# Kernel optimization log

Hardware: AMD Instinct MI355X
Metric: run time of the kernel (lower is better)

Reference implementation:

```python
import jax, jax.numpy as jnp
import numpy as np

LR, HR = 1024, 2048
H1, D1 = 8, (2 * HR) // 8   # feature_learner: heads=8, head_dim=512, out=2*HR
H2, D2 = 4, HR // 4          # upsampler: heads=4, head_dim=512, out=HR
EPS = 1e-5


def _graph_norm(h, gamma, beta, mscale):
    # PyG GraphNorm over a single graph: mean/var across the node dimension.
    mean = h.mean(axis=0, keepdims=True)
    out = h - mscale * mean
    var = (out * out).mean(axis=0, keepdims=True)
    return gamma * out * jax.lax.rsqrt(var + EPS) + beta


def _l2norm_rows(h):
    return h / jnp.linalg.norm(h, axis=1, keepdims=True)


def _transformer_conv(x, Wq, bq, Wk, bk, Wv, bv, Wskip, bskip, H, D, We=None, e=None):
    # PyG TransformerConv on a complete graph (with self-loops) == dense MHA
    # with optional scalar edge feature e[i, j] embedded via We and added to
    # key and value, plus a root/skip linear term.
    N = x.shape[0]
    Q = (x @ Wq + bq).reshape(N, H, D)
    K = (x @ Wk + bk).reshape(N, H, D)
    V = (x @ Wv + bv).reshape(N, H, D)
    scores = jnp.einsum('ihd,jhd->hij', Q, K)  # [H, N, N]
    if We is not None:
        Weh = We.reshape(H, D)                              # edge embedding dirs
        qe = jnp.einsum('ihd,hd->hi', Q, Weh)               # q_i . We per head
        scores = scores + qe[:, :, None] * e[None]          # + e_ij * (q.We)
    alpha = jax.nn.softmax(scores / jnp.sqrt(jnp.float32(D)), axis=2)
    out = jnp.einsum('hij,jhd->ihd', alpha, V)              # [N, H, D]
    if We is not None:
        ae = jnp.einsum('hij,ij->ih', alpha, e)             # sum_j alpha*e_ij
        out = out + ae[:, :, None] * Weh[None]
    return out.reshape(N, H * D) + x @ Wskip + bskip


def setup_inputs() -> dict:
    key = jax.random.key(0)
    ks = jax.random.split(key, 24)
    s_in = 1.0 / np.sqrt(LR)
    s_e = 1.0

    def p(k, shape, scale):
        return (jax.random.normal(k, shape, jnp.float32) * scale)

    F1 = H1 * D1  # 4096
    F2 = H2 * D2  # 2048
    return {
        'x': jax.random.normal(ks[0], (LR, LR), jnp.float32),
        # conv1 (feature_learner): in=LR, out=F1, edge_dim=1
        'Wq1': p(ks[1], (LR, F1), s_in), 'bq1': jnp.zeros((F1,), jnp.float32),
        'Wk1': p(ks[2], (LR, F1), s_in), 'bk1': jnp.zeros((F1,), jnp.float32),
        'Wv1': p(ks[3], (LR, F1), s_in), 'bv1': jnp.zeros((F1,), jnp.float32),
        'We1': p(ks[4], (1, F1), s_e),
        'Wskip1': p(ks[5], (LR, F1), s_in), 'bskip1': jnp.zeros((F1,), jnp.float32),
        'g1': jnp.ones((F1,), jnp.float32), 'bb1': jnp.zeros((F1,), jnp.float32),
        'ms1': jnp.ones((F1,), jnp.float32),
        # conv2 (upsampler): in=LR, out=F2, no edge features
        'Wq2': p(ks[6], (LR, F2), s_in), 'bq2': jnp.zeros((F2,), jnp.float32),
        'Wk2': p(ks[7], (LR, F2), s_in), 'bk2': jnp.zeros((F2,), jnp.float32),
        'Wv2': p(ks[8], (LR, F2), s_in), 'bv2': jnp.zeros((F2,), jnp.float32),
        'Wskip2': p(ks[9], (LR, F2), s_in), 'bskip2': jnp.zeros((F2,), jnp.float32),
        'g2': jnp.ones((F2,), jnp.float32), 'bb2': jnp.zeros((F2,), jnp.float32),
        'ms2': jnp.ones((F2,), jnp.float32),
    }


def reference(x, Wq1, bq1, Wk1, bk1, Wv1, bv1, We1, Wskip1, bskip1, g1, bb1, ms1,
              Wq2, bq2, Wk2, bk2, Wv2, bv2, Wskip2, bskip2, g2, bb2, ms2):
    # feature learner: edge_attr = x.view(-1,1), edge (src=j, dst=i) carries x[j, i]
    h1 = _transformer_conv(x, Wq1, bq1, Wk1, bk1, Wv1, bv1, Wskip1, bskip1,
                           H1, D1, We=We1, e=x.T)
    h1 = _graph_norm(h1, g1, bb1, ms1)
    lr_x = _l2norm_rows(h1)                      # [LR, 2*HR]
    # upsampler: nodes are the 2*HR columns of lr_x
    h2 = _transformer_conv(lr_x.T, Wq2, bq2, Wk2, bk2, Wv2, bv2, Wskip2, bskip2,
                           H2, D2)               # [2*HR, HR]
    hr_x = _graph_norm(h2, g2, bb2, ms2).T       # [HR, 2*HR]
    hr_x = _l2norm_rows(hr_x)
    hr = jax.nn.relu(hr_x @ hr_x.T)              # [HR, HR]
    return (hr, jax.nn.relu(lr_x @ lr_x.T))
```

## Files before the change

### kernel.cpp

```cpp
#include <hip/hip_runtime.h>
#include <hip/hip_bf16.h>

typedef unsigned short u16;
typedef __attribute__((ext_vector_type(8))) short bf16x8;
typedef __attribute__((ext_vector_type(4))) float f32x4;

__device__ __constant__ float kInvSqrtD = 0.04419417382415922f;

__device__ __forceinline__ u16 f2bf(float f) {
  union { float f; unsigned u; } a; a.f = f;
  unsigned r = a.u + 0x7FFFu + ((a.u >> 16) & 1u);
  return (u16)(r >> 16);
}
__device__ __forceinline__ float bf2f(u16 u) {
  union { unsigned u; float f; } a; a.u = ((unsigned)u) << 16;
  return a.f;
}

__device__ __forceinline__ float blockReduceMax(float v, float* red) {
  int tid = threadIdx.x;
  red[tid] = v; __syncthreads();
  #pragma unroll
  for (int w = 128; w > 0; w >>= 1) {
    if (tid < w) red[tid] = fmaxf(red[tid], red[tid + w]);
    __syncthreads();
  }
  float r = red[0];
  __syncthreads();
  return r;
}
__device__ __forceinline__ float blockReduceSum(float v, float* red) {
  int tid = threadIdx.x;
  red[tid] = v; __syncthreads();
  #pragma unroll
  for (int w = 128; w > 0; w >>= 1) {
    if (tid < w) red[tid] = red[tid] + red[tid + w];
    __syncthreads();
  }
  float r = red[0];
  __syncthreads();
  return r;
}

__device__ __forceinline__ float4 blockReduceF4(float4 v, float4* red) {
  int tid = threadIdx.x;
  red[tid] = v; __syncthreads();
  #pragma unroll
  for (int w = 128; w > 0; w >>= 1) {
    if (tid < w) {
      float4 a = red[tid], b = red[tid + w];
      a.x += b.x; a.y += b.y; a.z += b.z; a.w += b.w;
      red[tid] = a;
    }
    __syncthreads();
  }
  float4 r = red[0];
  __syncthreads();
  return r;
}

#define GLDS16(gp, lp)                                                         \
  __builtin_amdgcn_global_load_lds(                                            \
      (const __attribute__((address_space(1))) void*)(gp),                     \
      (__attribute__((address_space(3))) void*)(lp), 16, 0, 0)

__device__ __forceinline__ void xcd_map(int gx, int gy, int& bx, int& by) {
  const int nwg = gx * gy;
  const int orig = blockIdx.y * gx + blockIdx.x;
  if ((nwg & 7) == 0) {
    int bestfx = 0, bestcost = 1 << 30;
    #pragma unroll
    for (int fx = 1; fx <= 8; fx <<= 1) {
      int fy = 8 / fx;
      if ((gx % fx) == 0 && (gy % fy) == 0) {
        int cost = gx / fx + gy / fy;
        if (cost < bestcost) { bestcost = cost; bestfx = fx; }
      }
    }
    if (bestfx > 0) {
      const int fx = bestfx, fy = 8 / bestfx;
      const int rw = gx / fx, rh = gy / fy;
      const int xcd = orig & 7, lid = orig >> 3;
      bx = (xcd % fx) * rw + lid % rw;
      by = (xcd / fx) * rh + lid / rw;
      return;
    }
    const int q = nwg >> 3;
    const int xcd = orig & 7, lid = orig >> 3;
    const int wgid = xcd * q + lid;
    bx = wgid % gx; by = wgid / gx;
    return;
  }
  const int q = nwg >> 3, r = nwg & 7;
  const int xcd = orig & 7, lid = orig >> 3;
  const int wgid = (xcd < r ? xcd * (q + 1) : r * (q + 1) + (xcd - r) * q) + lid;
  bx = wgid % gx; by = wgid / gx;
}

template<int OUTM, bool ACCUM, bool RELU, bool RANK1, bool BIAS>
__global__ __launch_bounds__(512) void mgemm8_k(
    const u16* __restrict__ A, int lda, long long sA,
    const u16* __restrict__ B, int ldb, long long sB,
    const float* __restrict__ bias, int sBias,
    float* __restrict__ Cf, u16* __restrict__ Cb, int ldc, long long sC,
    int K,
    const float* __restrict__ r1row, int sR1r,
    const float* __restrict__ r1col, int sR1c)
{
  __shared__ u16 smem[8 * 8192];
  const int z = blockIdx.z;
  const u16* Ag = A + (long long)z * sA;
  const u16* Bg = B + (long long)z * sB;

  int bx, by;
  xcd_map(gridDim.x, gridDim.y, bx, by);

  const int row0 = by << 7;
  const int col0 = bx << 7;
  const int tid  = threadIdx.x;
  const int lane = tid & 63;
  const int w    = tid >> 6;
  const int g    = w >> 2;
  const int s4   = w & 3;
  const int wr   = (s4 >> 1) << 6;
  const int wc   = (s4 & 1) << 6;

  const int srow = tid >> 2;
  const int ssw  = (tid & 3) ^ ((srow >> 1) & 3);
  const long long aoff = (long long)(row0 + srow) * lda + ssw * 8;
  const long long boff = (long long)(col0 + srow) * ldb + ssw * 8;

  const int frow = lane & 15;
  const int fsw  = (lane >> 4) ^ ((frow >> 1) & 3);
  const int fAoff = ((wr + frow) << 5) + (fsw << 3);
  const int fBoff = ((wc + frow) << 5) + (fsw << 3);

#define STAGE8(tt) do {                                                        \
    u16* _sb = smem + (((tt) & 7) << 13);                                      \
    const long long _k = (long long)(tt) << 5;                                 \
    GLDS16(Ag + aoff + _k, _sb + (tid << 3));                                  \
    GLDS16(Bg + boff + _k, _sb + 4096 + (tid << 3));                           \
  } while (0)

  f32x4 acc[4][4];
  #pragma unroll
  for (int mi = 0; mi < 4; ++mi)
    #pragma unroll
    for (int ni = 0; ni < 4; ++ni) {
      acc[mi][ni][0] = 0.f; acc[mi][ni][1] = 0.f;
      acc[mi][ni][2] = 0.f; acc[mi][ni][3] = 0.f;
    }

  const int NT = K >> 5;
  const int NP = NT >> 1;
  STAGE8(0); STAGE8(1); STAGE8(2); STAGE8(3); STAGE8(4); STAGE8(5);
  asm volatile("s_waitcnt vmcnt(8)" ::: "memory");
  __builtin_amdgcn_s_barrier();
  asm volatile("" ::: "memory");

  for (int i = 0; i < NP; ++i) {
    if (i + 3 < NP) { STAGE8(2 * i + 6); STAGE8(2 * i + 7); }

    const u16* base = smem + (((2 * i + g) & 7) << 13);
    bf16x8 af[4], bfr[4];
    #pragma unroll
    for (int mi = 0; mi < 4; ++mi) af[mi]  = *(const bf16x8*)(base + fAoff + mi * 512);
    #pragma unroll
    for (int ni = 0; ni < 4; ++ni) bfr[ni] = *(const bf16x8*)(base + 4096 + fBoff + ni * 512);
    __builtin_amdgcn_s_setprio(1);
    #pragma unroll
    for (int mi = 0; mi < 4; ++mi)
      #pragma unroll
      for (int ni = 0; ni < 4; ++ni)
        acc[mi][ni] = __builtin_amdgcn_mfma_f32_16x16x32_bf16(
            af[mi], bfr[ni], acc[mi][ni], 0, 0, 0);
    __builtin_amdgcn_s_setprio(0);

    if (i + 1 < NP) {
      if (i + 3 < NP)      asm volatile("s_waitcnt vmcnt(8)" ::: "memory");
      else if (i + 2 < NP) asm volatile("s_waitcnt vmcnt(4)" ::: "memory");
      else                 asm volatile("s_waitcnt vmcnt(0)" ::: "memory");
      __builtin_amdgcn_s_barrier();
      asm volatile("" ::: "memory");
    }
  }
#undef STAGE8

  float* dump = (float*)smem;
  if (w >= 4) {
    float* reg = dump + ((w - 4) << 12);
    #pragma unroll
    for (int f = 0; f < 16; ++f) {
      int mi = f >> 2, ni = f & 3;
      *(f32x4*)(reg + (lane << 6) + (((f + lane) & 15) << 2)) = acc[mi][ni];
    }
  }
  asm volatile("s_waitcnt lgkmcnt(0)" ::: "memory");
  __builtin_amdgcn_s_barrier();
  asm volatile("" ::: "memory");
  if (w < 4) {
    float* reg = dump + (w << 12);
    #pragma unroll
    for (int f = 0; f < 16; ++f) {
      int mi = f >> 2, ni = f & 3;
      acc[mi][ni] += *(const f32x4*)(reg + (lane << 6) + (((f + lane) & 15) << 2));
    }
  }
  asm volatile("s_waitcnt lgkmcnt(0)" ::: "memory");
  __builtin_amdgcn_s_barrier();
  asm volatile("" ::: "memory");

  float* tile = (float*)smem;
  if (w < 4) {
    const int cn  = lane & 15;
    const int rm4 = (lane >> 4) << 2;
    #pragma unroll
    for (int mi = 0; mi < 4; ++mi) {
      #pragma unroll
      for (int ni = 0; ni < 4; ++ni) {
        const int rl = wr + mi * 16 + rm4;
        const int cl = wc + ni * 16 + cn;
        if (OUTM == 2) {
          *(f32x4*)&tile[cl * 132 + rl] = acc[mi][ni];
        } else {
          #pragma unroll
          for (int j = 0; j < 4; ++j) tile[(rl + j) * 132 + cl] = acc[mi][ni][j];
        }
      }
    }
  }
  asm volatile("s_waitcnt lgkmcnt(0)" ::: "memory");
  __builtin_amdgcn_s_barrier();
  asm volatile("" ::: "memory");

  #pragma unroll
  for (int p = 0; p < 8; ++p) {
    const int rr = p * 16 + (tid >> 5);
    const int c4 = (tid & 31) << 2;
    f32x4 v = *(const f32x4*)&tile[rr * 132 + c4];
    if (OUTM == 2) {
      const int cc = col0 + rr;
      float badd = BIAS ? bias[(long long)z * sBias + cc] : 0.f;
      u16* pp = Cb + (long long)z * sC + (long long)cc * ldc + row0 + c4;
      ushort4 o;
      o.x = f2bf(v[0] + badd); o.y = f2bf(v[1] + badd);
      o.z = f2bf(v[2] + badd); o.w = f2bf(v[3] + badd);
      *(ushort4*)pp = o;
    } else {
      const int R = row0 + rr;
      const long long idx = (long long)z * sC + (long long)R * ldc + col0 + c4;
      float val[4] = {v[0], v[1], v[2], v[3]};
      if (BIAS) {
        float4 b4 = *(const float4*)&bias[(long long)z * sBias + col0 + c4];
        val[0] += b4.x; val[1] += b4.y; val[2] += b4.z; val[3] += b4.w;
      }
      if (RANK1) {
        float rr1 = r1row[(long long)z * sR1r + R];
        float4 c4v = *(const float4*)&r1col[(long long)z * sR1c + col0 + c4];
        val[0] += rr1 * c4v.x; val[1] += rr1 * c4v.y;
        val[2] += rr1 * c4v.z; val[3] += rr1 * c4v.w;
      }
      if (OUTM == 0) {
        if (ACCUM) {
          float4 old = *(const float4*)&Cf[idx];
          val[0] += old.x; val[1] += old.y; val[2] += old.z; val[3] += old.w;
        }
        if (RELU) {
          val[0] = fmaxf(val[0], 0.f); val[1] = fmaxf(val[1], 0.f);
          val[2] = fmaxf(val[2], 0.f); val[3] = fmaxf(val[3], 0.f);
        }
        float4 o4; o4.x = val[0]; o4.y = val[1]; o4.z = val[2]; o4.w = val[3];
        *(float4*)&Cf[idx] = o4;
      } else {
        ushort4 o;
        o.x = f2bf(val[0]); o.y = f2bf(val[1]);
        o.z = f2bf(val[2]); o.w = f2bf(val[3]);
        *(ushort4*)&Cb[idx] = o;
      }
    }
  }
}

template<bool BIAS>
__global__ __launch_bounds__(512, 2) void mgemm256_k(
    const u16* __restrict__ A, int lda, long long sA,
    const u16* __restrict__ B, int ldb, long long sB,
    const float* __restrict__ bias, int sBias,
    u16* __restrict__ Cb, int ldc, long long sC,
    int K)
{
  __shared__ u16 smem[4 * 16384];
  const int z = blockIdx.z;
  const u16* Ag = A + (long long)z * sA;
  const u16* Bg = B + (long long)z * sB;

  int bx, by;
  xcd_map(gridDim.x, gridDim.y, bx, by);

  const int row0 = bx << 8;
  const int dummy = 0; (void)dummy;
  const int row0r = by << 8;
  const int col0 = bx << 8;
  (void)row0;
  const int tid  = threadIdx.x;
  const int lane = tid & 63;
  const int w    = tid >> 6;
  const int wrow = w >> 2;
  const int wcol = w & 3;

  const int srow = tid >> 2;
  const int ssw  = (tid & 3) ^ ((srow >> 1) & 3);
  const long long aoff0 = (long long)(row0r + srow)       * lda + ssw * 8;
  const long long aoff1 = (long long)(row0r + srow + 128) * lda + ssw * 8;
  const long long boff0 = (long long)(col0 + srow)        * ldb + ssw * 8;
  const long long boff1 = (long long)(col0 + srow + 128)  * ldb + ssw * 8;

  const int frow = lane & 15;
  const int fsw  = (lane >> 4) ^ ((frow >> 1) & 3);
  const int fAoff = ((wrow * 128 + frow) << 5) + (fsw << 3);
  const int fBoff = ((wcol * 64  + frow) << 5) + (fsw << 3);

#define STG256(tt) do {                                                        \
    u16* _sb = smem + (((tt) & 3) << 14);                                      \
    const long long _k = (long long)(tt) << 5;                                 \
    GLDS16(Ag + aoff0 + _k, _sb + (tid << 3));                                 \
    GLDS16(Ag + aoff1 + _k, _sb + 4096 + (tid << 3));                          \
    GLDS16(Bg + boff0 + _k, _sb + 8192 + (tid << 3));                          \
    GLDS16(Bg + boff1 + _k, _sb + 12288 + (tid << 3));                         \
  } while (0)

  f32x4 acc[8][4];
  #pragma unroll
  for (int mi = 0; mi < 8; ++mi)
    #pragma unroll
    for (int ni = 0; ni < 4; ++ni) {
      acc[mi][ni][0] = 0.f; acc[mi][ni][1] = 0.f;
      acc[mi][ni][2] = 0.f; acc[mi][ni][3] = 0.f;
    }

  const int NT = K >> 5;
  STG256(0); STG256(1); STG256(2);
  asm volatile("s_waitcnt vmcnt(8)" ::: "memory");
  __builtin_amdgcn_s_barrier();
  asm volatile("" ::: "memory");

  for (int t = 0; t < NT; ++t) {
    if (t + 3 < NT) STG256(t + 3);

    const u16* base = smem + ((t & 3) << 14);
    bf16x8 af[8], bfr[4];
    #pragma unroll
    for (int mi = 0; mi < 8; ++mi) af[mi]  = *(const bf16x8*)(base + fAoff + mi * 512);
    #pragma unroll
    for (int ni = 0; ni < 4; ++ni) bfr[ni] = *(const bf16x8*)(base + 8192 + fBoff + ni * 512);
    __builtin_amdgcn_s_setprio(1);
    #pragma unroll
    for (int mi = 0; mi < 8; ++mi)
      #pragma unroll
      for (int ni = 0; ni < 4; ++ni)
        acc[mi][ni] = __builtin_amdgcn_mfma_f32_16x16x32_bf16(
            af[mi], bfr[ni], acc[mi][ni], 0, 0, 0);
    __builtin_amdgcn_s_setprio(0);

    if (t + 1 < NT) {
      if (t + 3 < NT)      asm volatile("s_waitcnt vmcnt(8)" ::: "memory");
      else if (t + 2 < NT) asm volatile("s_waitcnt vmcnt(4)" ::: "memory");
      else                 asm volatile("s_waitcnt vmcnt(0)" ::: "memory");
      __builtin_amdgcn_s_barrier();
      asm volatile("" ::: "memory");
    }
  }
#undef STG256

  const int cn  = lane & 15;
  const int rm4 = (lane >> 4) << 2;
  #pragma unroll
  for (int mi = 0; mi < 8; ++mi) {
    #pragma unroll
    for (int ni = 0; ni < 4; ++ni) {
      const int rb = row0r + wrow * 128 + mi * 16 + rm4;
      const int cc = col0 + wcol * 64 + ni * 16 + cn;
      float badd = BIAS ? bias[(long long)z * sBias + cc] : 0.f;
      f32x4 v = acc[mi][ni];
      #pragma unroll
      for (int j = 0; j < 4; ++j)
        Cb[(long long)z * sC + (long long)(rb + j) * ldc + cc] = f2bf(v[j] + badd);
    }
  }
}

__global__ __launch_bounds__(256) void reduce4relu_k(
    const float* __restrict__ p, float* __restrict__ out, int n4)
{
  int i = blockIdx.x * 256 + threadIdx.x;
  if (i < n4) {
    float4 a = ((const float4*)p)[i];
    float4 b = ((const float4*)(p + (1ll << 20)))[i];
    float4 c = ((const float4*)(p + (2ll << 20)))[i];
    float4 d = ((const float4*)(p + (3ll << 20)))[i];
    float4 o;
    o.x = fmaxf(a.x + b.x + c.x + d.x, 0.f);
    o.y = fmaxf(a.y + b.y + c.y + d.y, 0.f);
    o.z = fmaxf(a.z + b.z + c.z + d.z, 0.f);
    o.w = fmaxf(a.w + b.w + c.w + d.w, 0.f);
    ((float4*)out)[i] = o;
  }
}

__global__ __launch_bounds__(256) void xpose_k(
    const float* __restrict__ in, float* __restrict__ out, int R, int Cc)
{
  __shared__ float tile[32][33];
  int c0 = blockIdx.x * 32, r0 = blockIdx.y * 32;
  int tx = threadIdx.x & 31, ty = threadIdx.x >> 5;
  #pragma unroll
  for (int rr = ty; rr < 32; rr += 8)
    tile[rr][tx] = in[(long long)(r0 + rr) * Cc + c0 + tx];
  __syncthreads();
  #pragma unroll
  for (int cc = ty; cc < 32; cc += 8)
    out[(long long)(c0 + cc) * R + r0 + tx] = tile[tx][cc];
}

__global__ __launch_bounds__(256) void tcvt_k(
    const float* __restrict__ in, u16* __restrict__ out, int R, int Cc)
{
  __shared__ float tile[32][33];
  int c0 = blockIdx.x * 32, r0 = blockIdx.y * 32;
  int tx = threadIdx.x & 31, ty = threadIdx.x >> 5;
  #pragma unroll
  for (int rr = ty; rr < 32; rr += 8)
    tile[rr][tx] = in[(long long)(r0 + rr) * Cc + c0 + tx];
  __syncthreads();
  #pragma unroll
  for (int cc = ty; cc < 32; cc += 8)
    out[(long long)(c0 + cc) * R + r0 + tx] = f2bf(tile[tx][cc]);
}

__global__ __launch_bounds__(256) void tcvt_aff_k(
    const float* __restrict__ in, u16* __restrict__ out, int R, int Cc,
    const float* __restrict__ A2, const float* __restrict__ C2)
{
  __shared__ float tile[32][33];
  int c0 = blockIdx.x * 32, r0 = blockIdx.y * 32;
  int tx = threadIdx.x & 31, ty = threadIdx.x >> 5;
  #pragma unroll
  for (int rr = ty; rr < 32; rr += 8)
    tile[rr][tx] = in[(long long)(r0 + rr) * Cc + c0 + tx];
  __syncthreads();
  #pragma unroll
  for (int cc = ty; cc < 32; cc += 8) {
    float v = A2[c0 + cc] * tile[tx][cc] + C2[c0 + cc];
    out[(long long)(c0 + cc) * R + r0 + tx] = f2bf(v);
  }
}

__global__ __launch_bounds__(256) void cvt_k(
    const float* __restrict__ in, u16* __restrict__ out)
{
  int i = blockIdx.x * 256 + threadIdx.x;
  float4 v = ((const float4*)in)[i];
  ushort4 o;
  o.x = f2bf(v.x); o.y = f2bf(v.y); o.z = f2bf(v.z); o.w = f2bf(v.w);
  ((ushort4*)out)[i] = o;
}

__global__ __launch_bounds__(256) void pack2_k(
    const float* __restrict__ a, const float* __restrict__ b,
    float* __restrict__ out, int n)
{
  int i = blockIdx.x * 256 + threadIdx.x;
  if (i < n) { out[i] = a[i]; out[n + i] = b[i]; }
}

__global__ __launch_bounds__(64) void qe_k(const u16* __restrict__ Q1,
                                           const float* __restrict__ We1,
                                           float* __restrict__ qe)
{
  int h = blockIdx.x >> 10;
  int i = blockIdx.x & 1023;
  const u16* q = Q1 + (long long)i * 4096 + h * 512;
  const float* wv = We1 + h * 512;
  int l = threadIdx.x;
  float s = 0.f;
  #pragma unroll
  for (int r = 0; r < 8; ++r) s += bf2f(q[l + r * 64]) * wv[l + r * 64];
  #pragma unroll
  for (int off = 32; off > 0; off >>= 1) s += __shfl_down(s, off);
  if (l == 0) qe[blockIdx.x] = s;
}

__global__ __launch_bounds__(256) void softmax1b_k(
    u16* __restrict__ S, const float* __restrict__ xT,
    const float* __restrict__ qe, float* __restrict__ ae)
{
  int i = blockIdx.x, h = blockIdx.y;
  u16* s = S + ((long long)h * 1024 + i) * 1024;
  const float* e = xT + (long long)i * 1024;
  float q = qe[h * 1024 + i];
  int tid = threadIdx.x;
  __shared__ float red[256];

  ushort4 sv = ((const ushort4*)s)[tid];
  float4  evv = ((const float4*)e)[tid];
  float ev[4] = {evv.x, evv.y, evv.z, evv.w};
  float t[4];
  t[0] = (bf2f(sv.x) + q * ev[0]) * kInvSqrtD;
  t[1] = (bf2f(sv.y) + q * ev[1]) * kInvSqrtD;
  t[2] = (bf2f(sv.z) + q * ev[2]) * kInvSqrtD;
  t[3] = (bf2f(sv.w) + q * ev[3]) * kInvSqrtD;
  float m = fmaxf(fmaxf(t[0], t[1]), fmaxf(t[2], t[3]));
  m = blockReduceMax(m, red);
  float sum = 0.f;
  #pragma unroll
  for (int r = 0; r < 4; ++r) { t[r] = __expf(t[r] - m); sum += t[r]; }
  sum = blockReduceSum(sum, red);
  float invl = 1.f / sum;
  float aes = 0.f;
  ushort4 o;
  o.x = f2bf(t[0] * invl); o.y = f2bf(t[1] * invl);
  o.z = f2bf(t[2] * invl); o.w = f2bf(t[3] * invl);
  #pragma unroll
  for (int r = 0; r < 4; ++r) aes += (t[r] * invl) * ev[r];
  ((ushort4*)s)[tid] = o;
  aes = blockReduceSum(aes, red);
  if (tid == 0) ae[h * 1024 + i] = aes;
}

__global__ __launch_bounds__(256) void softmax2b_k(u16* __restrict__ S)
{
  u16* s = S + ((long long)blockIdx.y * 2048 + blockIdx.x) * 4096;
  int tid = threadIdx.x;
  __shared__ float red[256];
  float t[16];
  float m = -1e30f;
  #pragma unroll
  for (int r = 0; r < 4; ++r) {
    ushort4 sv = ((const ushort4*)s)[tid + r * 256];
    t[r*4+0] = bf2f(sv.x) * kInvSqrtD; t[r*4+1] = bf2f(sv.y) * kInvSqrtD;
    t[r*4+2] = bf2f(sv.z) * kInvSqrtD; t[r*4+3] = bf2f(sv.w) * kInvSqrtD;
    m = fmaxf(m, fmaxf(fmaxf(t[r*4], t[r*4+1]), fmaxf(t[r*4+2], t[r*4+3])));
  }
  m = blockReduceMax(m, red);
  float sum = 0.f;
  #pragma unroll
  for (int r = 0; r < 16; ++r) { t[r] = __expf(t[r] - m); sum += t[r]; }
  sum = blockReduceSum(sum, red);
  float invl = 1.f / sum;
  #pragma unroll
  for (int r = 0; r < 4; ++r) {
    ushort4 o;
    o.x = f2bf(t[r*4+0] * invl); o.y = f2bf(t[r*4+1] * invl);
    o.z = f2bf(t[r*4+2] * invl); o.w = f2bf(t[r*4+3] * invl);
    ((ushort4*)s)[tid + r * 256] = o;
  }
}

__global__ __launch_bounds__(256) void colpart4_k(const float* __restrict__ h,
    int N, int F, int nchunk, float* __restrict__ ps, float* __restrict__ pss)
{
  const int f4 = blockIdx.x * 256 + threadIdx.x;
  const int chunk = blockIdx.y;
  const int rows = N / nchunk;
  const int rbeg = chunk * rows;
  const int F4 = F >> 2;
  const float4* h4 = (const float4*)h;
  float4 s = {0.f, 0.f, 0.f, 0.f}, ss = {0.f, 0.f, 0.f, 0.f};
  #pragma unroll 8
  for (int i = 0; i < rows; ++i) {
    float4 v = h4[(long long)(rbeg + i) * F4 + f4];
    s.x += v.x; s.y += v.y; s.z += v.z; s.w += v.w;
    ss.x += v.x * v.x; ss.y += v.y * v.y;
    ss.z += v.z * v.z; ss.w += v.w * v.w;
  }
  ((float4*)(ps  + (long long)chunk * F))[f4] = s;
  ((float4*)(pss + (long long)chunk * F))[f4] = ss;
}

template<int MODE>
__global__ __launch_bounds__(256) void colfin2_k(
    const float* __restrict__ ps, const float* __restrict__ pss,
    int F, int nchunk, float Nf,
    const float* __restrict__ ms, const float* __restrict__ g,
    const float* __restrict__ beta,
    float* __restrict__ outA, float* __restrict__ outC)
{
  __shared__ float4 red4[256];
  const int f4 = blockIdx.x;
  const int tid = threadIdx.x;
  float4 s = {0.f, 0.f, 0.f, 0.f}, ss = {0.f, 0.f, 0.f, 0.f};
  for (int c = tid; c < nchunk; c += 256) {
    float4 v = ((const float4*)(ps  + (long long)c * F))[f4];
    float4 u = ((const float4*)(pss + (long long)c * F))[f4];
    s.x += v.x; s.y += v.y; s.z += v.z; s.w += v.w;
    ss.x += u.x; ss.y += u.y; ss.z += u.z; ss.w += u.w;
  }
  s  = blockReduceF4(s, red4);
  ss = blockReduceF4(ss, red4);
  if (tid < 4) {
    const int f = f4 * 4 + tid;
    float sv  = (tid == 0) ? s.x  : (tid == 1) ? s.y  : (tid == 2) ? s.z  : s.w;
    float ssv = (tid == 0) ? ss.x : (tid == 1) ? ss.y : (tid == 2) ? ss.z : ss.w;
    float Ninv = 1.f / Nf;
    float mean = sv * Ninv;
    float mm = ms[f] * mean;
    float var = ssv * Ninv - 2.f * mm * mean + mm * mm;
    float is = rsqrtf(var + 1e-5f);
    float a = g[f] * is;
    float c = beta[f] - a * mm;
    if (MODE == 1) {
      float sy2 = a * a * ssv + 2.f * a * c * sv + Nf * c * c;
      float cinv = rsqrtf(sy2);
      a *= cinv; c *= cinv;
    }
    outA[f] = a;
    outC[f] = c;
  }
}

__global__ __launch_bounds__(256) void rowl2gn_k(
    float* __restrict__ h, u16* __restrict__ hb,
    const float* __restrict__ a, const float* __restrict__ c)
{
  int i = blockIdx.x;
  float* row = h + (long long)i * 4096;
  u16* rb = hb + (long long)i * 4096;
  int tid = threadIdx.x;
  __shared__ float red[256];
  float t[16];
  float ss = 0.f;
  #pragma unroll
  for (int r = 0; r < 4; ++r) {
    int j = tid + r * 256;
    float4 hv = ((const float4*)row)[j];
    float4 av = ((const float4*)a)[j];
    float4 cv = ((const float4*)c)[j];
    t[r*4+0] = av.x * hv.x + cv.x;
    t[r*4+1] = av.y * hv.y + cv.y;
    t[r*4+2] = av.z * hv.z + cv.z;
    t[r*4+3] = av.w * hv.w + cv.w;
    ss += t[r*4+0]*t[r*4+0] + t[r*4+1]*t[r*4+1]
        + t[r*4+2]*t[r*4+2] + t[r*4+3]*t[r*4+3];
  }
  ss = blockReduceSum(ss, red);
  float inv = rsqrtf(ss);
  #pragma unroll
  for (int r = 0; r < 4; ++r) {
    int j = tid + r * 256;
    float4 o4;
    o4.x = t[r*4+0] * inv; o4.y = t[r*4+1] * inv;
    o4.z = t[r*4+2] * inv; o4.w = t[r*4+3] * inv;
    ((float4*)row)[j] = o4;
    ushort4 ob;
    ob.x = f2bf(o4.x); ob.y = f2bf(o4.y); ob.z = f2bf(o4.z); ob.w = f2bf(o4.w);
    ((ushort4*)rb)[j] = ob;
  }
}

extern "C" void kernel_launch(void* const* d_in, const int* in_sizes, int n_in,
                              void* d_out, int out_size, void* d_ws, size_t ws_size,
                              hipStream_t stream)
{
  (void)in_sizes; (void)n_in; (void)out_size; (void)ws_size;

  const float* x      = (const float*)d_in[0];
  const float* Wq1    = (const float*)d_in[1];
  const float* bq1    = (const float*)d_in[2];
  const float* Wk1    = (const float*)d_in[3];
  const float* bk1    = (const float*)d_in[4];
  const float* Wv1    = (const float*)d_in[5];
  const float* bv1    = (const float*)d_in[6];
  const float* We1    = (const float*)d_in[7];
  const float* Wskip1 = (const float*)d_in[8];
  const float* bskip1 = (const float*)d_in[9];
  const float* g1     = (const float*)d_in[10];
  const float* bb1    = (const float*)d_in[11];
  const float* ms1    = (const float*)d_in[12];
  const float* Wq2    = (const float*)d_in[13];
  const float* bq2    = (const float*)d_in[14];
  const float* Wk2    = (const float*)d_in[15];
  const float* bk2    = (const float*)d_in[16];
  const float* Wv2    = (const float*)d_in[17];
  const float* bv2    = (const float*)d_in[18];
  const float* Wskip2 = (const float*)d_in[19];
  const float* bskip2 = (const float*)d_in[20];
  const float* g2     = (const float*)d_in[21];
  const float* bb2    = (const float*)d_in[22];
  const float* ms2    = (const float*)d_in[23];

  char* base = (char*)d_ws;
  float* lrx_f   = (float*)(base);
  u16*   lrx_bf  = (u16*)  (base + (16ll << 20));
  u16*   lrxT_bf = (u16*)  (base + (24ll << 20));
  u16*   hrx_bf  = (u16*)  (base + (32ll << 20));
  char* sh = base + (48ll << 20);
  u16* x_bf  = (u16*)(sh);
  float* xT  = (float*)(sh + (2ll << 20));
  u16* Wq1T  = (u16*)(sh + (6ll << 20));
  u16* Wk1T  = (u16*)(sh + (14ll << 20));
  u16* Wv1T  = (u16*)(sh + (22ll << 20));
  u16* Ws1T  = (u16*)(sh + (30ll << 20));
  u16* Q1bf  = (u16*)(sh + (38ll << 20));
  u16* K1bf  = (u16*)(sh + (46ll << 20));
  u16* V1T   = (u16*)(sh + (54ll << 20));
  u16* S1bf  = (u16*)(sh + (62ll << 20));
  float* ps1  = (float*)(sh + (66ll << 20));
  float* pss1 = (float*)(sh + (68ll << 20));
  u16* Wq2T  = (u16*)(sh);
  u16* Wk2T  = (u16*)(sh + (4ll << 20));
  u16* Wv2T  = (u16*)(sh + (8ll << 20));
  u16* Ws2T  = (u16*)(sh + (12ll << 20));
  u16* Q2bf  = (u16*)(sh + (16ll << 20));
  u16* K2bf  = (u16*)(sh + (32ll << 20));
  u16* V2T   = (u16*)(sh + (48ll << 20));
  float* H2  = (float*)(sh + (64ll << 20));
  u16* S2bf  = (u16*)(sh + (96ll << 20));
  float* gpart = (float*)(sh + (96ll << 20));
  float* ps2  = (float*)(sh + (120ll << 20));
  float* pss2 = (float*)(sh + (122ll << 20));
  float* tail    = (float*)(base + (208ll << 20));
  float* qe      = tail;
  float* ae      = qe + 8192;
  float* af1     = ae + 8192;
  float* cf1     = af1 + 4096;
  float* A2v     = cf1 + 4096;
  float* C2v     = A2v + 2048;
  float* biasQK1 = C2v + 2048;
  float* biasQK2 = biasQK1 + 8192;

  float* out0 = (float*)d_out;
  float* out1 = out0 + (long long)2048 * 2048;

  xpose_k<<<dim3(32, 32), 256, 0, stream>>>(x, xT, 1024, 1024);
  cvt_k<<<dim3(1024), 256, 0, stream>>>(x, x_bf);
  tcvt_k<<<dim3(128, 32), 256, 0, stream>>>(Wq1,    Wq1T, 1024, 4096);
  tcvt_k<<<dim3(128, 32), 256, 0, stream>>>(Wk1,    Wk1T, 1024, 4096);
  tcvt_k<<<dim3(128, 32), 256, 0, stream>>>(Wv1,    Wv1T, 1024, 4096);
  tcvt_k<<<dim3(128, 32), 256, 0, stream>>>(Wskip1, Ws1T, 1024, 4096);
  pack2_k<<<dim3(16), 256, 0, stream>>>(bq1, bk1, biasQK1, 4096);
  pack2_k<<<dim3(8),  256, 0, stream>>>(bq2, bk2, biasQK2, 2048);

  mgemm8_k<1,false,false,false,true><<<dim3(32, 8, 2), 512, 0, stream>>>(
      x_bf, 1024, 0, Wq1T, 1024, (long long)4096 * 1024, biasQK1, 4096,
      nullptr, Q1bf, 4096, (long long)1024 * 4096, 1024, nullptr, 0, nullptr, 0);
  mgemm8_k<2,false,false,false,true><<<dim3(32, 8, 1), 512, 0, stream>>>(
      x_bf, 1024, 0, Wv1T, 1024, 0, bv1, 0, nullptr, V1T, 1024, 0, 1024,
      nullptr, 0, nullptr, 0);
  mgemm8_k<0,false,false,false,true><<<dim3(32, 8, 1), 512, 0, stream>>>(
      x_bf, 1024, 0, Ws1T, 1024, 0, bskip1, 0, lrx_f, nullptr, 4096, 0, 1024,
      nullptr, 0, nullptr, 0);

  qe_k<<<dim3(8192), 64, 0, stream>>>(Q1bf, We1, qe);

  mgemm8_k<1,false,false,false,false><<<dim3(8, 8, 8), 512, 0, stream>>>(
      Q1bf, 4096, 512, K1bf, 4096, 512, nullptr, 0, nullptr, S1bf, 1024, 1048576,
      512, nullptr, 0, nullptr, 0);

  softmax1b_k<<<dim3(1024, 8), 256, 0, stream>>>(S1bf, xT, qe, ae);

  mgemm8_k<0,true,false,true,false><<<dim3(4, 8, 8), 512, 0, stream>>>(
      S1bf, 1024, 1048576, V1T, 1024, 512 * 1024, nullptr, 0, lrx_f, nullptr,
      4096, 512, 1024, ae, 1024, We1, 512);

  colpart4_k<<<dim3(4, 128), 256, 0, stream>>>(lrx_f, 1024, 4096, 128, ps1, pss1);
  colfin2_k<0><<<dim3(1024), 256, 0, stream>>>(ps1, pss1, 4096, 128, 1024.f,
                                               ms1, g1, bb1, af1, cf1);
  rowl2gn_k<<<dim3(1024), 256, 0, stream>>>(lrx_f, lrx_bf, af1, cf1);
  tcvt_k<<<dim3(128, 32), 256, 0, stream>>>(lrx_f, lrxT_bf, 1024, 4096);

  tcvt_k<<<dim3(64, 32), 256, 0, stream>>>(Wq2,    Wq2T, 1024, 2048);
  tcvt_k<<<dim3(64, 32), 256, 0, stream>>>(Wk2,    Wk2T, 1024, 2048);
  tcvt_k<<<dim3(64, 32), 256, 0, stream>>>(Wv2,    Wv2T, 1024, 2048);
  tcvt_k<<<dim3(64, 32), 256, 0, stream>>>(Wskip2, Ws2T, 1024, 2048);

  mgemm256_k<true><<<dim3(8, 16, 2), 512, 0, stream>>>(
      lrxT_bf, 1024, 0, Wq2T, 1024, (long long)2048 * 1024, biasQK2, 2048,
      Q2bf, 2048, (long long)4096 * 2048, 1024);
  mgemm8_k<2,false,false,false,true><<<dim3(16, 32, 1), 512, 0, stream>>>(
      lrxT_bf, 1024, 0, Wv2T, 1024, 0, bv2, 0, nullptr, V2T, 4096, 0, 1024,
      nullptr, 0, nullptr, 0);
  mgemm8_k<0,false,false,false,true><<<dim3(16, 32, 1), 512, 0, stream>>>(
      lrxT_bf, 1024, 0, Ws2T, 1024, 0, bskip2, 0, H2, nullptr, 2048, 0, 1024,
      nullptr, 0, nullptr, 0);

  for (int c = 0; c < 2; ++c) {
    const u16* Qc = Q2bf + (long long)c * 2048 * 2048;
    float* Hc = H2 + (long long)c * 2048 * 2048;
    mgemm256_k<false><<<dim3(16, 8, 4), 512, 0, stream>>>(
        Qc, 2048, 512, K2bf, 2048, 512, nullptr, 0,
        S2bf, 4096, (long long)2048 * 4096, 512);
    softmax2b_k<<<dim3(2048, 4), 256, 0, stream>>>(S2bf);
    mgemm8_k<0,true,false,false,false><<<dim3(4, 16, 4), 512, 0, stream>>>(
        S2bf, 4096, (long long)2048 * 4096, V2T, 4096, (long long)512 * 4096,
        nullptr, 0, Hc, nullptr, 2048, 512, 4096, nullptr, 0, nullptr, 0);
  }

  colpart4_k<<<dim3(2, 256), 256, 0, stream>>>(H2, 4096, 2048, 256, ps2, pss2);
  colfin2_k<1><<<dim3(512), 256, 0, stream>>>(ps2, pss2, 2048, 256, 4096.f,
                                              ms2, g2, bb2, A2v, C2v);
  tcvt_aff_k<<<dim3(64, 128), 256, 0, stream>>>(H2, hrx_bf, 4096, 2048, A2v, C2v);

  mgemm8_k<0,false,true,false,false><<<dim3(16, 16, 1), 512, 0, stream>>>(
      hrx_bf, 4096, 0, hrx_bf, 4096, 0, nullptr, 0, out0, nullptr, 2048, 0, 4096,
      nullptr, 0, nullptr, 0);
  mgemm8_k<0,false,false,false,false><<<dim3(8, 8, 4), 512, 0, stream>>>(
      lrx_bf, 4096, 1024, lrx_bf, 4096, 1024, nullptr, 0, gpart, nullptr, 1024,
      (long long)1 << 20, 1024, nullptr, 0, nullptr, 0);
  reduce4relu_k<<<dim3(1024), 256, 0, stream>>>(gpart, out1, 262144);
}
```

Measured before the change: 644.3 us.

## Shrink GEMM shared-memory rings to raise occupancy with double-barrier pipelining

Both GEMM kernels now keep fewer shared-memory stages: 4 stages instead of 8 for the 128-tile kernel and 2 instead of 4 for the 256-tile kernel. Each now declares launch_bounds(512,4) so more workgroups can be resident per CU. The loop reads fragments into registers first, then hits a second barrier, then issues the next global-to-LDS loads so they overlap the MFMAs. The epilogue is factored into a shared helper. In exchange there is a shallower prefetch depth, an extra barrier per iteration, and a tighter register budget that may cause spills.

```diff
diff --git a/kernel.cpp b/kernel.cpp
--- a/kernel.cpp
+++ b/kernel.cpp
@@ -98,94 +98,13 @@
 }
 
 template<int OUTM, bool ACCUM, bool RELU, bool RANK1, bool BIAS>
-__global__ __launch_bounds__(512) void mgemm8_k(
-    const u16* __restrict__ A, int lda, long long sA,
-    const u16* __restrict__ B, int ldb, long long sB,
-    const float* __restrict__ bias, int sBias,
-    float* __restrict__ Cf, u16* __restrict__ Cb, int ldc, long long sC,
-    int K,
-    const float* __restrict__ r1row, int sR1r,
-    const float* __restrict__ r1col, int sR1c)
-{
-  __shared__ u16 smem[8 * 8192];
-  const int z = blockIdx.z;
-  const u16* Ag = A + (long long)z * sA;
-  const u16* Bg = B + (long long)z * sB;
-
-  int bx, by;
-  xcd_map(gridDim.x, gridDim.y, bx, by);
-
-  const int row0 = by << 7;
-  const int col0 = bx << 7;
-  const int tid  = threadIdx.x;
-  const int lane = tid & 63;
-  const int w    = tid >> 6;
-  const int g    = w >> 2;
-  const int s4   = w & 3;
-  const int wr   = (s4 >> 1) << 6;
-  const int wc   = (s4 & 1) << 6;
-
-  const int srow = tid >> 2;
-  const int ssw  = (tid & 3) ^ ((srow >> 1) & 3);
-  const long long aoff = (long long)(row0 + srow) * lda + ssw * 8;
-  const long long boff = (long long)(col0 + srow) * ldb + ssw * 8;
-
-  const int frow = lane & 15;
-  const int fsw  = (lane >> 4) ^ ((frow >> 1) & 3);
-  const int fAoff = ((wr + frow) << 5) + (fsw << 3);
-  const int fBoff = ((wc + frow) << 5) + (fsw << 3);
-
-#define STAGE8(tt) do {                                                        \
-    u16* _sb = smem + (((tt) & 7) << 13);                                      \
-    const long long _k = (long long)(tt) << 5;                                 \
-    GLDS16(Ag + aoff + _k, _sb + (tid << 3));                                  \
-    GLDS16(Bg + boff + _k, _sb + 4096 + (tid << 3));                           \
-  } while (0)
-
-  f32x4 acc[4][4];
-  #pragma unroll
-  for (int mi = 0; mi < 4; ++mi)
-    #pragma unroll
-    for (int ni = 0; ni < 4; ++ni) {
-      acc[mi][ni][0] = 0.f; acc[mi][ni][1] = 0.f;
-      acc[mi][ni][2] = 0.f; acc[mi][ni][3] = 0.f;
-    }
-
-  const int NT = K >> 5;
-  const int NP = NT >> 1;
-  STAGE8(0); STAGE8(1); STAGE8(2); STAGE8(3); STAGE8(4); STAGE8(5);
-  asm volatile("s_waitcnt vmcnt(8)" ::: "memory");
-  __builtin_amdgcn_s_barrier();
-  asm volatile("" ::: "memory");
-
-  for (int i = 0; i < NP; ++i) {
-    if (i + 3 < NP) { STAGE8(2 * i + 6); STAGE8(2 * i + 7); }
-
-    const u16* base = smem + (((2 * i + g) & 7) << 13);
-    bf16x8 af[4], bfr[4];
-    #pragma unroll
-    for (int mi = 0; mi < 4; ++mi) af[mi]  = *(const bf16x8*)(base + fAoff + mi * 512);
-    #pragma unroll
-    for (int ni = 0; ni < 4; ++ni) bfr[ni] = *(const bf16x8*)(base + 4096 + fBoff + ni * 512);
-    __builtin_amdgcn_s_setprio(1);
-    #pragma unroll
-    for (int mi = 0; mi < 4; ++mi)
-      #pragma unroll
-      for (int ni = 0; ni < 4; ++ni)
-        acc[mi][ni] = __builtin_amdgcn_mfma_f32_16x16x32_bf16(
-            af[mi], bfr[ni], acc[mi][ni], 0, 0, 0);
-    __builtin_amdgcn_s_setprio(0);
-
-    if (i + 1 < NP) {
-      if (i + 3 < NP)      asm volatile("s_waitcnt vmcnt(8)" ::: "memory");
-      else if (i + 2 < NP) asm volatile("s_waitcnt vmcnt(4)" ::: "memory");
-      else                 asm volatile("s_waitcnt vmcnt(0)" ::: "memory");
-      __builtin_amdgcn_s_barrier();
-      asm volatile("" ::: "memory");
-    }
-  }
-#undef STAGE8
-
+__device__ __forceinline__ void epilogue128(
+    u16* smem, f32x4 (&acc)[4][4],
+    int z, int row0, int col0, int tid, int lane, int w, int wr, int wc,
+    const float* bias, int sBias,
+    float* Cf, u16* Cb, int ldc, long long sC,
+    const float* r1row, int sR1r, const float* r1col, int sR1c)
+{
   float* dump = (float*)smem;
   if (w >= 4) {
     float* reg = dump + ((w - 4) << 12);
@@ -281,15 +200,107 @@
   }
 }
 
+template<int OUTM, bool ACCUM, bool RELU, bool RANK1, bool BIAS>
+__global__ __launch_bounds__(512, 4) void mgemm8d_k(
+    const u16* __restrict__ A, int lda, long long sA,
+    const u16* __restrict__ B, int ldb, long long sB,
+    const float* __restrict__ bias, int sBias,
+    float* __restrict__ Cf, u16* __restrict__ Cb, int ldc, long long sC,
+    int K,
+    const float* __restrict__ r1row, int sR1r,
+    const float* __restrict__ r1col, int sR1c)
+{
+  __shared__ u16 smem[33792];
+  const int z = blockIdx.z;
+  const u16* Ag = A + (long long)z * sA;
+  const u16* Bg = B + (long long)z * sB;
+
+  int bx, by;
+  xcd_map(gridDim.x, gridDim.y, bx, by);
+
+  const int row0 = by << 7;
+  const int col0 = bx << 7;
+  const int tid  = threadIdx.x;
+  const int lane = tid & 63;
+  const int w    = tid >> 6;
+  const int g    = w >> 2;
+  const int s4   = w & 3;
+  const int wr   = (s4 >> 1) << 6;
+  const int wc   = (s4 & 1) << 6;
+
+  const int srow = tid >> 2;
+  const int ssw  = (tid & 3) ^ ((srow >> 1) & 3);
+  const long long aoff = (long long)(row0 + srow) * lda + ssw * 8;
+  const long long boff = (long long)(col0 + srow) * ldb + ssw * 8;
+
+  const int frow = lane & 15;
+  const int fsw  = (lane >> 4) ^ ((frow >> 1) & 3);
+  const int fAoff = ((wr + frow) << 5) + (fsw << 3);
+  const int fBoff = ((wc + frow) << 5) + (fsw << 3);
+
+#define STAGE4(tt) do {                                                        \
+    u16* _sb = smem + (((tt) & 3) << 13);                                      \
+    const long long _k = (long long)(tt) << 5;                                 \
+    GLDS16(Ag + aoff + _k, _sb + (tid << 3));                                  \
+    GLDS16(Bg + boff + _k, _sb + 4096 + (tid << 3));                           \
+  } while (0)
+
+  f32x4 acc[4][4];
+  #pragma unroll
+  for (int mi = 0; mi < 4; ++mi)
+    #pragma unroll
+    for (int ni = 0; ni < 4; ++ni) {
+      acc[mi][ni][0] = 0.f; acc[mi][ni][1] = 0.f;
+      acc[mi][ni][2] = 0.f; acc[mi][ni][3] = 0.f;
+    }
+
+  const int NT = K >> 5;
+  const int NP = NT >> 1;
+  STAGE4(0); STAGE4(1); STAGE4(2); STAGE4(3);
+
+  for (int p = 0; p < NP; ++p) {
+    if (p + 1 < NP) asm volatile("s_waitcnt vmcnt(4)" ::: "memory");
+    else            asm volatile("s_waitcnt vmcnt(0)" ::: "memory");
+    __builtin_amdgcn_s_barrier();
+    asm volatile("" ::: "memory");
+
+    const u16* base = smem + (((2 * p + g) & 3) << 13);
+    bf16x8 af[4], bfr[4];
+    #pragma unroll
+    for (int mi = 0; mi < 4; ++mi) af[mi]  = *(const bf16x8*)(base + fAoff + mi * 512);
+    #pragma unroll
+    for (int ni = 0; ni < 4; ++ni) bfr[ni] = *(const bf16x8*)(base + 4096 + fBoff + ni * 512);
+    asm volatile("s_waitcnt lgkmcnt(0)" ::: "memory");
+    __builtin_amdgcn_s_barrier();
+    asm volatile("" ::: "memory");
+
+    if (p + 2 < NP) { STAGE4(2 * p + 4); STAGE4(2 * p + 5); }
+
+    __builtin_amdgcn_s_setprio(1);
+    #pragma unroll
+    for (int mi = 0; mi < 4; ++mi)
+      #pragma unroll
+      for (int ni = 0; ni < 4; ++ni)
+        acc[mi][ni] = __builtin_amdgcn_mfma_f32_16x16x32_bf16(
+            af[mi], bfr[ni], acc[mi][ni], 0, 0, 0);
+    __builtin_amdgcn_s_setprio(0);
+  }
+#undef STAGE4
+
+  epilogue128<OUTM, ACCUM, RELU, RANK1, BIAS>(
+      smem, acc, z, row0, col0, tid, lane, w, wr, wc,
+      bias, sBias, Cf, Cb, ldc, sC, r1row, sR1r, r1col, sR1c);
+}
+
 template<bool BIAS>
-__global__ __launch_bounds__(512, 2) void mgemm256_k(
+__global__ __launch_bounds__(512, 4) void mgemm256d_k(
     const u16* __restrict__ A, int lda, long long sA,
     const u16* __restrict__ B, int ldb, long long sB,
     const float* __restrict__ bias, int sBias,
     u16* __restrict__ Cb, int ldc, long long sC,
     int K)
 {
-  __shared__ u16 smem[4 * 16384];
+  __shared__ u16 smem[2 * 16384];
   const int z = blockIdx.z;
   const u16* Ag = A + (long long)z * sA;
   const u16* Bg = B + (long long)z * sB;
@@ -297,11 +308,8 @@
   int bx, by;
   xcd_map(gridDim.x, gridDim.y, bx, by);
 
-  const int row0 = bx << 8;
-  const int dummy = 0; (void)dummy;
   const int row0r = by << 8;
   const int col0 = bx << 8;
-  (void)row0;
   const int tid  = threadIdx.x;
   const int lane = tid & 63;
   const int w    = tid >> 6;
@@ -321,7 +329,7 @@
   const int fBoff = ((wcol * 64  + frow) << 5) + (fsw << 3);
 
 #define STG256(tt) do {                                                        \
-    u16* _sb = smem + (((tt) & 3) << 14);                                      \
+    u16* _sb = smem + (((tt) & 1) << 14);                                      \
     const long long _k = (long long)(tt) << 5;                                 \
     GLDS16(Ag + aoff0 + _k, _sb + (tid << 3));                                 \
     GLDS16(Ag + aoff1 + _k, _sb + 4096 + (tid << 3));                          \
@@ -339,20 +347,26 @@
     }
 
   const int NT = K >> 5;
-  STG256(0); STG256(1); STG256(2);
-  asm volatile("s_waitcnt vmcnt(8)" ::: "memory");
-  __builtin_amdgcn_s_barrier();
-  asm volatile("" ::: "memory");
+  STG256(0); STG256(1);
 
   for (int t = 0; t < NT; ++t) {
-    if (t + 3 < NT) STG256(t + 3);
-
-    const u16* base = smem + ((t & 3) << 14);
+    if (t + 1 < NT) asm volatile("s_waitcnt vmcnt(4)" ::: "memory");
+    else            asm volatile("s_waitcnt vmcnt(0)" ::: "memory");
+    __builtin_amdgcn_s_barrier();
+    asm volatile("" ::: "memory");
+
+    const u16* base = smem + ((t & 1) << 14);
     bf16x8 af[8], bfr[4];
     #pragma unroll
     for (int mi = 0; mi < 8; ++mi) af[mi]  = *(const bf16x8*)(base + fAoff + mi * 512);
     #pragma unroll
     for (int ni = 0; ni < 4; ++ni) bfr[ni] = *(const bf16x8*)(base + 8192 + fBoff + ni * 512);
+    asm volatile("s_waitcnt lgkmcnt(0)" ::: "memory");
+    __builtin_amdgcn_s_barrier();
+    asm volatile("" ::: "memory");
+
+    if (t + 2 < NT) STG256(t + 2);
+
     __builtin_amdgcn_s_setprio(1);
     #pragma unroll
     for (int mi = 0; mi < 8; ++mi)
@@ -361,14 +375,6 @@
         acc[mi][ni] = __builtin_amdgcn_mfma_f32_16x16x32_bf16(
             af[mi], bfr[ni], acc[mi][ni], 0, 0, 0);
     __builtin_amdgcn_s_setprio(0);
-
-    if (t + 1 < NT) {
-      if (t + 3 < NT)      asm volatile("s_waitcnt vmcnt(8)" ::: "memory");
-      else if (t + 2 < NT) asm volatile("s_waitcnt vmcnt(4)" ::: "memory");
-      else                 asm volatile("s_waitcnt vmcnt(0)" ::: "memory");
-      __builtin_amdgcn_s_barrier();
-      asm volatile("" ::: "memory");
-    }
   }
 #undef STG256
 
@@ -740,25 +746,25 @@
   pack2_k<<<dim3(16), 256, 0, stream>>>(bq1, bk1, biasQK1, 4096);
   pack2_k<<<dim3(8),  256, 0, stream>>>(bq2, bk2, biasQK2, 2048);
 
-  mgemm8_k<1,false,false,false,true><<<dim3(32, 8, 2), 512, 0, stream>>>(
+  mgemm8d_k<1,false,false,false,true><<<dim3(32, 8, 2), 512, 0, stream>>>(
       x_bf, 1024, 0, Wq1T, 1024, (long long)4096 * 1024, biasQK1, 4096,
       nullptr, Q1bf, 4096, (long long)1024 * 4096, 1024, nullptr, 0, nullptr, 0);
-  mgemm8_k<2,false,false,false,true><<<dim3(32, 8, 1), 512, 0, stream>>>(
+  mgemm8d_k<2,false,false,false,true><<<dim3(32, 8, 1), 512, 0, stream>>>(
       x_bf, 1024, 0, Wv1T, 1024, 0, bv1, 0, nullptr, V1T, 1024, 0, 1024,
       nullptr, 0, nullptr, 0);
-  mgemm8_k<0,false,false,false,true><<<dim3(32, 8, 1), 512, 0, stream>>>(
+  mgemm8d_k<0,false,false,false,true><<<dim3(32, 8, 1), 512, 0, stream>>>(
       x_bf, 1024, 0, Ws1T, 1024, 0, bskip1, 0, lrx_f, nullptr, 4096, 0, 1024,
       nullptr, 0, nullptr, 0);
 
   qe_k<<<dim3(8192), 64, 0, stream>>>(Q1bf, We1, qe);
 
-  mgemm8_k<1,false,false,false,false><<<dim3(8, 8, 8), 512, 0, stream>>>(
+  mgemm8d_k<1,false,false,false,false><<<dim3(8, 8, 8), 512, 0, stream>>>(
       Q1bf, 4096, 512, K1bf, 4096, 512, nullptr, 0, nullptr, S1bf, 1024, 1048576,
       512, nullptr, 0, nullptr, 0);
 
   softmax1b_k<<<dim3(1024, 8), 256, 0, stream>>>(S1bf, xT, qe, ae);
 
-  mgemm8_k<0,true,false,true,false><<<dim3(4, 8, 8), 512, 0, stream>>>(
+  mgemm8d_k<0,true,false,true,false><<<dim3(4, 8, 8), 512, 0, stream>>>(
       S1bf, 1024, 1048576, V1T, 1024, 512 * 1024, nullptr, 0, lrx_f, nullptr,
       4096, 512, 1024, ae, 1024, We1, 512);
 
@@ -773,24 +779,24 @@
   tcvt_k<<<dim3(64, 32), 256, 0, stream>>>(Wv2,    Wv2T, 1024, 2048);
   tcvt_k<<<dim3(64, 32), 256, 0, stream>>>(Wskip2, Ws2T, 1024, 2048);
 
-  mgemm256_k<true><<<dim3(8, 16, 2), 512, 0, stream>>>(
+  mgemm256d_k<true><<<dim3(8, 16, 2), 512, 0, stream>>>(
       lrxT_bf, 1024, 0, Wq2T, 1024, (long long)2048 * 1024, biasQK2, 2048,
       Q2bf, 2048, (long long)4096 * 2048, 1024);
-  mgemm8_k<2,false,false,false,true><<<dim3(16, 32, 1), 512, 0, stream>>>(
+  mgemm8d_k<2,false,false,false,true><<<dim3(16, 32, 1), 512, 0, stream>>>(
       lrxT_bf, 1024, 0, Wv2T, 1024, 0, bv2, 0, nullptr, V2T, 4096, 0, 1024,
       nullptr, 0, nullptr, 0);
-  mgemm8_k<0,false,false,false,true><<<dim3(16, 32, 1), 512, 0, stream>>>(
+  mgemm8d_k<0,false,false,false,true><<<dim3(16, 32, 1), 512, 0, stream>>>(
       lrxT_bf, 1024, 0, Ws2T, 1024, 0, bskip2, 0, H2, nullptr, 2048, 0, 1024,
       nullptr, 0, nullptr, 0);
 
   for (int c = 0; c < 2; ++c) {
     const u16* Qc = Q2bf + (long long)c * 2048 * 2048;
     float* Hc = H2 + (long long)c * 2048 * 2048;
-    mgemm256_k<false><<<dim3(16, 8, 4), 512, 0, stream>>>(
+    mgemm256d_k<false><<<dim3(16, 8, 4), 512, 0, stream>>>(
         Qc, 2048, 512, K2bf, 2048, 512, nullptr, 0,
         S2bf, 4096, (long long)2048 * 4096, 512);
     softmax2b_k<<<dim3(2048, 4), 256, 0, stream>>>(S2bf);
-    mgemm8_k<0,true,false,false,false><<<dim3(4, 16, 4), 512, 0, stream>>>(
+    mgemm8d_k<0,true,false,false,false><<<dim3(4, 16, 4), 512, 0, stream>>>(
         S2bf, 4096, (long long)2048 * 4096, V2T, 4096, (long long)512 * 4096,
         nullptr, 0, Hc, nullptr, 2048, 512, 4096, nullptr, 0, nullptr, 0);
   }
@@ -800,10 +806,10 @@
                                               ms2, g2, bb2, A2v, C2v);
   tcvt_aff_k<<<dim3(64, 128), 256, 0, stream>>>(H2, hrx_bf, 4096, 2048, A2v, C2v);
 
-  mgemm8_k<0,false,true,false,false><<<dim3(16, 16, 1), 512, 0, stream>>>(
+  mgemm8d_k<0,false,true,false,false><<<dim3(16, 16, 1), 512, 0, stream>>>(
       hrx_bf, 4096, 0, hrx_bf, 4096, 0, nullptr, 0, out0, nullptr, 2048, 0, 4096,
       nullptr, 0, nullptr, 0);
-  mgemm8_k<0,false,false,false,false><<<dim3(8, 8, 4), 512, 0, stream>>>(
+  mgemm8d_k<0,false,false,false,false><<<dim3(8, 8, 4), 512, 0, stream>>>(
       lrx_bf, 4096, 1024, lrx_bf, 4096, 1024, nullptr, 0, gpart, nullptr, 1024,
       (long long)1 << 20, 1024, nullptr, 0, nullptr, 0);
   reduce4relu_k<<<dim3(1024), 256, 0, stream>>>(gpart, out1, 262144);
```

After: 1.628 ms. +152.7%, slower.
